# Optimization experiments

Hardware: AMD Instinct MI355X
Metric: run time of the kernel (lower is better)

Reference implementation:

```python
import jax, jax.numpy as jnp
import numpy as np

N, E, D, H, C, HID, ED = 50000, 800000, 128, 8, 16, 512, 32


def setup_inputs() -> dict:
    key = jax.random.key(0)
    ks = jax.random.split(key, 16)
    s = 0.05
    return {
        "h": jax.random.normal(ks[0], (N, D), jnp.float32),
        "edge_index": jax.random.randint(ks[1], (2, E), 0, N, jnp.int64),
        "edge_attr": jax.random.normal(ks[2], (E, ED), jnp.float32),
        "w1": jax.random.normal(ks[3], (D, HID), jnp.float32) * s,
        "b1": jnp.zeros((HID,), jnp.float32),
        "w2": jax.random.normal(ks[4], (HID, D), jnp.float32) * s,
        "b2": jnp.zeros((D,), jnp.float32),
        "ln_g": jnp.ones((D,), jnp.float32),
        "ln_b": jnp.zeros((D,), jnp.float32),
        "Wl": jax.random.normal(ks[5], (D, H * C), jnp.float32) * s,
        "bl": jnp.zeros((H * C,), jnp.float32),
        "Wr": jax.random.normal(ks[6], (D, H * C), jnp.float32) * s,
        "br": jnp.zeros((H * C,), jnp.float32),
        "We": jax.random.normal(ks[7], (ED, H * C), jnp.float32) * s,
        "att": jax.random.normal(ks[8], (H, C), jnp.float32) * s,
        "bias_out": jnp.zeros((H * C,), jnp.float32),
    }


def _layer_norm(x, g, b, eps=1e-5):
    mu = jnp.mean(x, axis=-1, keepdims=True)
    var = jnp.var(x, axis=-1, keepdims=True)
    return (x - mu) * jax.lax.rsqrt(var + eps) * g + b


def reference(h, edge_index, edge_attr, w1, b1, w2, b2, ln_g, ln_b,
              Wl, bl, Wr, br, We, att, bias_out):
    # FFN + residual + LayerNorm (dropout = identity in eval)
    u = jax.nn.relu(h @ w1 + b1) @ w2 + b2
    v = _layer_norm(h + u, ln_g, ln_b)

    src, dst = edge_index[0], edge_index[1]
    # GATv2Conv: separate source/target transforms + edge transform
    xl = (v @ Wl + bl).reshape(N, H, C)
    xr = (v @ Wr + br).reshape(N, H, C)
    xe = (edge_attr @ We).reshape(E, H, C)
    x = jax.nn.leaky_relu(xl[src] + xr[dst] + xe, 0.2)  # [E,H,C]
    logits = jnp.einsum("ehc,hc->eh", x, att)            # [E,H]
    # segment softmax over incoming edges of each destination node
    m = jax.lax.stop_gradient(jax.ops.segment_max(logits, dst, num_segments=N))
    ex = jnp.exp(logits - m[dst])
    den = jax.ops.segment_sum(ex, dst, num_segments=N)
    alpha = ex / den[dst]                                # [E,H]
    msg = xl[src] * alpha[..., None]                     # [E,H,C]
    w = jax.ops.segment_sum(msg, dst, num_segments=N).reshape(N, H * C) + bias_out
    output = _layer_norm(w + v, ln_g, ln_b)
    return output, alpha
```

## Files before the change

kernel.cpp:

```cpp
#include <hip/hip_runtime.h>
#include <math.h>

#define N_NODES 50000
#define E_EDGES 800000
#define D_DIM   128
#define H_HEADS 8
#define C_CH    16
#define HID_DIM 512
#define ED_DIM  32

typedef __attribute__((ext_vector_type(8))) short short8;
typedef __attribute__((ext_vector_type(4))) float f32x4;

__device__ __forceinline__ short f2bf(float f) {
    unsigned u = __float_as_uint(f);
    return (short)((u + 0x7FFFu + ((u >> 16) & 1u)) >> 16);
}
__device__ __forceinline__ float bf2f(short s) {
    return __uint_as_float(((unsigned)(unsigned short)s) << 16);
}

__global__ __launch_bounds__(64) void repack_kernel(
    const float* __restrict__ w1, const float* __restrict__ w2,
    const float* __restrict__ Wl, const float* __restrict__ Wr,
    const float* __restrict__ We,
    short8* __restrict__ w1p, short8* __restrict__ w2p,
    short8* __restrict__ Wlp, short8* __restrict__ Wrp,
    short8* __restrict__ Wep)
{
    int b = blockIdx.x;
    const float* src; short8* dst; int Nw, nc, rel;
    if (b < 128)      { src = w1; dst = w1p; Nw = 512; nc = 4;  rel = b; }
    else if (b < 256) { src = w2; dst = w2p; Nw = 128; nc = 16; rel = b - 128; }
    else if (b < 288) { src = Wl; dst = Wlp; Nw = 128; nc = 4;  rel = b - 256; }
    else if (b < 320) { src = Wr; dst = Wrp; Nw = 128; nc = 4;  rel = b - 288; }
    else              { src = We; dst = Wep; Nw = 128; nc = 1;  rel = b - 320; }
    int t = rel / nc, c = rel % nc;
    int l = threadIdx.x, quad = l >> 4, col = l & 15;
    short8 r;
    #pragma unroll
    for (int j = 0; j < 8; ++j)
        r[j] = f2bf(src[(size_t)(c * 32 + quad * 8 + j) * Nw + t * 16 + col]);
    dst[(size_t)rel * 64 + l] = r;
}

__global__ __launch_bounds__(256) void node_ffn_mfma(
    const float* __restrict__ h,
    const float* __restrict__ b1, const float* __restrict__ b2,
    const float* __restrict__ ln_g, const float* __restrict__ ln_b,
    const float* __restrict__ bl, const float* __restrict__ br,
    const short8* __restrict__ w1p, const short8* __restrict__ w2p,
    const short8* __restrict__ Wlp, const short8* __restrict__ Wrp,
    float* __restrict__ v_out, float* __restrict__ xl_out, float* __restrict__ xr_out)
{
    __shared__ short hid_bf[16 * 520];
    __shared__ float v_s[16 * 132];
    __shared__ short v_bf[16 * 136];

    const int tid = threadIdx.x;
    const int w = tid >> 6, lane = tid & 63;
    const int m = lane & 15, quad = lane >> 4;
    const int n0 = blockIdx.x * 16;

    short8 af[4];
    #pragma unroll
    for (int c = 0; c < 4; ++c) {
        const float* hp = h + (size_t)(n0 + m) * 128 + c * 32 + quad * 8;
        float4 p0 = ((const float4*)hp)[0];
        float4 p1 = ((const float4*)hp)[1];
        short8 a;
        a[0] = f2bf(p0.x); a[1] = f2bf(p0.y); a[2] = f2bf(p0.z); a[3] = f2bf(p0.w);
        a[4] = f2bf(p1.x); a[5] = f2bf(p1.y); a[6] = f2bf(p1.z); a[7] = f2bf(p1.w);
        af[c] = a;
    }

    {
        f32x4 acc[8];
        #pragma unroll
        for (int t = 0; t < 8; ++t) acc[t] = (f32x4){0.f, 0.f, 0.f, 0.f};
        #pragma unroll
        for (int t = 0; t < 8; ++t) {
            int tile = w * 8 + t;
            #pragma unroll
            for (int c = 0; c < 4; ++c) {
                short8 bf = w1p[(size_t)(tile * 4 + c) * 64 + lane];
                acc[t] = __builtin_amdgcn_mfma_f32_16x16x32_bf16(af[c], bf, acc[t], 0, 0, 0);
            }
        }
        #pragma unroll
        for (int t = 0; t < 8; ++t) {
            int col = (w * 8 + t) * 16 + m;
            float bias = b1[col];
            #pragma unroll
            for (int r = 0; r < 4; ++r) {
                int row = quad * 4 + r;
                hid_bf[row * 520 + col] = f2bf(fmaxf(acc[t][r] + bias, 0.f));
            }
        }
    }
    __syncthreads();

    {
        f32x4 acc2[2];
        acc2[0] = (f32x4){0.f, 0.f, 0.f, 0.f};
        acc2[1] = (f32x4){0.f, 0.f, 0.f, 0.f};
        #pragma unroll 4
        for (int c = 0; c < 16; ++c) {
            short8 a = *(const short8*)&hid_bf[m * 520 + c * 32 + quad * 8];
            #pragma unroll
            for (int t = 0; t < 2; ++t) {
                short8 bf = w2p[(size_t)((w * 2 + t) * 16 + c) * 64 + lane];
                acc2[t] = __builtin_amdgcn_mfma_f32_16x16x32_bf16(a, bf, acc2[t], 0, 0, 0);
            }
        }
        #pragma unroll
        for (int t = 0; t < 2; ++t) {
            int col = (w * 2 + t) * 16 + m;
            float bias = b2[col];
            #pragma unroll
            for (int r = 0; r < 4; ++r) {
                int row = quad * 4 + r;
                v_s[row * 132 + col] = acc2[t][r] + bias + h[(size_t)(n0 + row) * 128 + col];
            }
        }
    }
    __syncthreads();

    {
        float g0 = ln_g[lane], g1 = ln_g[lane + 64];
        float be0 = ln_b[lane], be1 = ln_b[lane + 64];
        #pragma unroll
        for (int p = 0; p < 4; ++p) {
            int nd = w * 4 + p;
            float x0 = v_s[nd * 132 + lane], x1 = v_s[nd * 132 + lane + 64];
            float s = x0 + x1, ss = x0 * x0 + x1 * x1;
            #pragma unroll
            for (int off = 1; off < 64; off <<= 1) {
                s  += __shfl_xor(s, off);
                ss += __shfl_xor(ss, off);
            }
            float mu = s * (1.f / 128.f);
            float var = ss * (1.f / 128.f) - mu * mu;
            float rs = rsqrtf(var + 1e-5f);
            float y0 = (x0 - mu) * rs * g0 + be0;
            float y1 = (x1 - mu) * rs * g1 + be1;
            v_out[(size_t)(n0 + nd) * 128 + lane]      = y0;
            v_out[(size_t)(n0 + nd) * 128 + lane + 64] = y1;
            v_bf[nd * 136 + lane]      = f2bf(y0);
            v_bf[nd * 136 + lane + 64] = f2bf(y1);
        }
    }
    __syncthreads();

    {
        short8 af3[4];
        #pragma unroll
        for (int c = 0; c < 4; ++c)
            af3[c] = *(const short8*)&v_bf[m * 136 + c * 32 + quad * 8];
        f32x4 accl[2], accr[2];
        #pragma unroll
        for (int t = 0; t < 2; ++t) {
            accl[t] = (f32x4){0.f, 0.f, 0.f, 0.f};
            accr[t] = (f32x4){0.f, 0.f, 0.f, 0.f};
        }
        #pragma unroll
        for (int t = 0; t < 2; ++t) {
            int tile = w * 2 + t;
            #pragma unroll
            for (int c = 0; c < 4; ++c) {
                accl[t] = __builtin_amdgcn_mfma_f32_16x16x32_bf16(
                    af3[c], Wlp[(size_t)(tile * 4 + c) * 64 + lane], accl[t], 0, 0, 0);
                accr[t] = __builtin_amdgcn_mfma_f32_16x16x32_bf16(
                    af3[c], Wrp[(size_t)(tile * 4 + c) * 64 + lane], accr[t], 0, 0, 0);
            }
        }
        #pragma unroll
        for (int t = 0; t < 2; ++t) {
            int col = (w * 2 + t) * 16 + m;
            float bld = bl[col], brd = br[col];
            #pragma unroll
            for (int r = 0; r < 4; ++r) {
                int row = quad * 4 + r;
                xl_out[(size_t)(n0 + row) * 128 + col] = accl[t][r] + bld;
                xr_out[(size_t)(n0 + row) * 128 + col] = accr[t][r] + brd;
            }
        }
    }
}

__global__ __launch_bounds__(256) void edge_logits_mfma(
    const int* __restrict__ edge_index, const float* __restrict__ edge_attr,
    const short8* __restrict__ Wep, const float* __restrict__ att,
    const float* __restrict__ xl, const float* __restrict__ xr,
    float* __restrict__ logits_out, unsigned* __restrict__ cnt,
    unsigned short* __restrict__ rank)
{
    __shared__ short8 We_f[512];
    __shared__ short xe_s[64 * 136];
    const int tid = threadIdx.x;
    const int w = tid >> 6, lane = tid & 63;
    const int m = lane & 15, quad = lane >> 4;
    const int e0 = blockIdx.x * 64;

    We_f[tid]       = Wep[tid];
    We_f[tid + 256] = Wep[tid + 256];

    const float* eap = edge_attr + (size_t)(e0 + w * 16 + m) * 32 + quad * 8;
    float4 p0 = ((const float4*)eap)[0];
    float4 p1 = ((const float4*)eap)[1];
    short8 a;
    a[0] = f2bf(p0.x); a[1] = f2bf(p0.y); a[2] = f2bf(p0.z); a[3] = f2bf(p0.w);
    a[4] = f2bf(p1.x); a[5] = f2bf(p1.y); a[6] = f2bf(p1.z); a[7] = f2bf(p1.w);

    __syncthreads();

    f32x4 acc[8];
    #pragma unroll
    for (int t = 0; t < 8; ++t) acc[t] = (f32x4){0.f, 0.f, 0.f, 0.f};
    #pragma unroll
    for (int t = 0; t < 8; ++t)
        acc[t] = __builtin_amdgcn_mfma_f32_16x16x32_bf16(a, We_f[t * 64 + lane], acc[t], 0, 0, 0);

    #pragma unroll
    for (int t = 0; t < 8; ++t) {
        #pragma unroll
        for (int r = 0; r < 4; ++r)
            xe_s[(w * 16 + quad * 4 + r) * 136 + t * 16 + m] = f2bf(acc[t][r]);
    }
    __syncthreads();

    const int g = quad;
    const int s = m;
    const int d0 = s * 8;
    float4 at0 = ((const float4*)(att + d0))[0];
    float4 at1 = ((const float4*)(att + d0))[1];

    #pragma unroll
    for (int p = 0; p < 4; ++p) {
        int el = p * 16 + w * 4 + g;
        int e = e0 + el;
        int src = edge_index[e];
        int dst = edge_index[E_EDGES + e];
        const float4* xlp = (const float4*)(xl + (size_t)src * 128 + d0);
        const float4* xrp = (const float4*)(xr + (size_t)dst * 128 + d0);
        float4 a0 = xlp[0], a1 = xlp[1];
        float4 r0 = xrp[0], r1 = xrp[1];
        short8 xe8 = *(const short8*)&xe_s[el * 136 + d0];

        float xv[8] = { a0.x + r0.x + bf2f(xe8[0]), a0.y + r0.y + bf2f(xe8[1]),
                        a0.z + r0.z + bf2f(xe8[2]), a0.w + r0.w + bf2f(xe8[3]),
                        a1.x + r1.x + bf2f(xe8[4]), a1.y + r1.y + bf2f(xe8[5]),
                        a1.z + r1.z + bf2f(xe8[6]), a1.w + r1.w + bf2f(xe8[7]) };
        float atv[8] = { at0.x, at0.y, at0.z, at0.w, at1.x, at1.y, at1.z, at1.w };
        float pq = 0.f;
        #pragma unroll
        for (int dd = 0; dd < 8; ++dd) {
            float x = xv[dd];
            x = (x > 0.f) ? x : 0.2f * x;
            pq += x * atv[dd];
        }
        pq += __shfl_xor(pq, 1);
        if ((s & 1) == 0)
            logits_out[(size_t)e * 8 + (s >> 1)] = pq;
        if (s == 0) {
            unsigned rk = atomicAdd(&cnt[dst], 1u);
            rank[e] = (unsigned short)rk;
        }
    }
}

__global__ __launch_bounds__(1024) void scan_kernel(
    const unsigned* __restrict__ cnt, int* __restrict__ rowstart)
{
    __shared__ int wsum[16];
    __shared__ int s_carry;
    const int t = threadIdx.x, wv = t >> 6, lane = t & 63;
    if (t == 0) s_carry = 0;
    __syncthreads();
    for (int base = 0; base < N_NODES; base += 1024) {
        int i = base + t;
        int v = (i < N_NODES) ? (int)cnt[i] : 0;
        int s = v;
        #pragma unroll
        for (int off = 1; off < 64; off <<= 1) {
            int nb = __shfl_up(s, off);
            if (lane >= off) s += nb;
        }
        if (lane == 63) wsum[wv] = s;
        __syncthreads();
        int woff = s_carry;
        for (int k = 0; k < wv; ++k) woff += wsum[k];
        if (i < N_NODES) rowstart[i] = woff + s - v;
        int tot = woff + s;
        __syncthreads();
        if (t == 1023) s_carry = tot;
    }
}

__global__ __launch_bounds__(256) void scatter_kernel(
    const int* __restrict__ edge_index, const unsigned short* __restrict__ rank,
    const int* __restrict__ rowstart, int* __restrict__ eidx)
{
    int e = blockIdx.x * 256 + threadIdx.x;
    if (e >= E_EDGES) return;
    int dst = edge_index[E_EDGES + e];
    eidx[rowstart[dst] + (int)rank[e]] = e;
}

__global__ __launch_bounds__(256) void node_aggregate_kernel(
    const int* __restrict__ eidx, const int* __restrict__ rowstart,
    const unsigned* __restrict__ cnt, const int* __restrict__ edge_index,
    const float* __restrict__ xl, const float* __restrict__ v,
    const float* __restrict__ bias_out,
    const float* __restrict__ ln_g, const float* __restrict__ ln_b,
    float* __restrict__ alphabuf, float* __restrict__ out)
{
    const int wv = threadIdx.x >> 6, lane = threadIdx.x & 63;
    const int n = blockIdx.x * 4 + wv;
    if (n >= N_NODES) return;
    const int start = rowstart[n];
    const int num = (int)cnt[n];

    const int hh = lane & 7;
    const int slot = lane >> 3;

    float den = 0.f;
    for (int i = slot; i < num; i += 8) {
        int e = eidx[start + i];
        den += expf(alphabuf[(size_t)e * 8 + hh]);
    }
    den += __shfl_xor(den, 8);
    den += __shfl_xor(den, 16);
    den += __shfl_xor(den, 32);
    float inv = 1.f / den;

    const int g = lane >> 4, s = lane & 15;
    const int h3 = s >> 1;
    float iv3 = __shfl(inv, h3);
    float acc[8] = {0.f, 0.f, 0.f, 0.f, 0.f, 0.f, 0.f, 0.f};
    for (int i = 0; i < num; i += 4) {
        int ii = i + g;
        if (ii < num) {
            int e = eidx[start + ii];
            int src = edge_index[e];
            float lg = alphabuf[(size_t)e * 8 + h3];
            float al = expf(lg) * iv3;
            if ((s & 1) == 0) alphabuf[(size_t)e * 8 + h3] = al;
            const float4* xp = (const float4*)(xl + (size_t)src * 128 + s * 8);
            float4 q0 = xp[0], q1 = xp[1];
            acc[0] += q0.x * al; acc[1] += q0.y * al;
            acc[2] += q0.z * al; acc[3] += q0.w * al;
            acc[4] += q1.x * al; acc[5] += q1.y * al;
            acc[6] += q1.z * al; acc[7] += q1.w * al;
        }
    }
    #pragma unroll
    for (int k = 0; k < 8; ++k) {
        acc[k] += __shfl_xor(acc[k], 16);
        acc[k] += __shfl_xor(acc[k], 32);
    }

    const float* vp = v + (size_t)n * 128 + s * 8;
    float4 v0 = ((const float4*)vp)[0], v1 = ((const float4*)vp)[1];
    float4 b0 = ((const float4*)(bias_out + s * 8))[0];
    float4 b1 = ((const float4*)(bias_out + s * 8))[1];
    float x[8];
    x[0] = acc[0] + b0.x + v0.x; x[1] = acc[1] + b0.y + v0.y;
    x[2] = acc[2] + b0.z + v0.z; x[3] = acc[3] + b0.w + v0.w;
    x[4] = acc[4] + b1.x + v1.x; x[5] = acc[5] + b1.y + v1.y;
    x[6] = acc[6] + b1.z + v1.z; x[7] = acc[7] + b1.w + v1.w;
    float sm = 0.f, ssm = 0.f;
    #pragma unroll
    for (int k = 0; k < 8; ++k) { sm += x[k]; ssm += x[k] * x[k]; }
    #pragma unroll
    for (int off = 1; off < 16; off <<= 1) {
        sm  += __shfl_xor(sm, off);
        ssm += __shfl_xor(ssm, off);
    }
    float mu = sm * (1.f / 128.f);
    float var = ssm * (1.f / 128.f) - mu * mu;
    float rs = rsqrtf(var + 1e-5f);
    if (g == 0) {
        float4 g0 = ((const float4*)(ln_g + s * 8))[0];
        float4 g1 = ((const float4*)(ln_g + s * 8))[1];
        float4 be0 = ((const float4*)(ln_b + s * 8))[0];
        float4 be1 = ((const float4*)(ln_b + s * 8))[1];
        float4 o0, o1;
        o0.x = (x[0] - mu) * rs * g0.x + be0.x;
        o0.y = (x[1] - mu) * rs * g0.y + be0.y;
        o0.z = (x[2] - mu) * rs * g0.z + be0.z;
        o0.w = (x[3] - mu) * rs * g0.w + be0.w;
        o1.x = (x[4] - mu) * rs * g1.x + be1.x;
        o1.y = (x[5] - mu) * rs * g1.y + be1.y;
        o1.z = (x[6] - mu) * rs * g1.z + be1.z;
        o1.w = (x[7] - mu) * rs * g1.w + be1.w;
        float4* op = (float4*)(out + (size_t)n * 128 + s * 8);
        op[0] = o0; op[1] = o1;
    }
}

extern "C" void kernel_launch(void* const* d_in, const int* in_sizes, int n_in,
                              void* d_out, int out_size, void* d_ws, size_t ws_size,
                              hipStream_t stream)
{
    const float* h        = (const float*)d_in[0];
    const int*   edge_idx = (const int*)  d_in[1];
    const float* edge_attr= (const float*)d_in[2];
    const float* w1       = (const float*)d_in[3];
    const float* b1       = (const float*)d_in[4];
    const float* w2       = (const float*)d_in[5];
    const float* b2       = (const float*)d_in[6];
    const float* ln_g     = (const float*)d_in[7];
    const float* ln_b     = (const float*)d_in[8];
    const float* Wl       = (const float*)d_in[9];
    const float* bl       = (const float*)d_in[10];
    const float* Wr       = (const float*)d_in[11];
    const float* br       = (const float*)d_in[12];
    const float* We       = (const float*)d_in[13];
    const float* att      = (const float*)d_in[14];
    const float* bias_out = (const float*)d_in[15];

    float* out   = (float*)d_out;
    float* alpha = out + (size_t)N_NODES * 128;

    short8* w1p = (short8*)alpha;
    short8* w2p = w1p + 128 * 64;
    short8* Wlp = w2p + 128 * 64;
    short8* Wrp = Wlp + 32 * 64;

    float*          v        = (float*)d_ws;
    float*          xl       = v  + (size_t)N_NODES * 128;
    float*          xr       = xl + (size_t)N_NODES * 128;
    unsigned*       cnt      = (unsigned*)(xr + (size_t)N_NODES * 128);
    int*            rowstart = (int*)(cnt + N_NODES);
    unsigned short* rank     = (unsigned short*)(rowstart + N_NODES);
    short8*         Wep      = (short8*)(rank + E_EDGES);
    int*            eidx     = (int*)xr;

    hipMemsetAsync(cnt, 0, (size_t)N_NODES * sizeof(unsigned), stream);

    repack_kernel<<<328, 64, 0, stream>>>(w1, w2, Wl, Wr, We,
                                          w1p, w2p, Wlp, Wrp, Wep);
    node_ffn_mfma<<<N_NODES / 16, 256, 0, stream>>>(
        h, b1, b2, ln_g, ln_b, bl, br, w1p, w2p, Wlp, Wrp, v, xl, xr);
    edge_logits_mfma<<<E_EDGES / 64, 256, 0, stream>>>(
        edge_idx, edge_attr, Wep, att, xl, xr, alpha, cnt, rank);
    scan_kernel<<<1, 1024, 0, stream>>>(cnt, rowstart);
    scatter_kernel<<<(E_EDGES + 255) / 256, 256, 0, stream>>>(
        edge_idx, rank, rowstart, eidx);
    node_aggregate_kernel<<<(N_NODES + 3) / 4, 256, 0, stream>>>(
        eidx, rowstart, cnt, edge_idx, xl, v, bias_out, ln_g, ln_b, alpha, out);
}
```

Measured before the change: 528.2 us.

## Build CSR before edge logits and process edges in destination-sorted order

Edge counting moves into a standalone count kernel ahead of the FFN, so the CSR (scan plus scatter) is built before the logits kernel. The logits kernel then walks edges in destination-sorted order using a packed 16-bit src/dst array, which should make the xr[dst] gathers hit cache. The aggregate kernel reads src from the contiguous packed array instead of gathering edge_index by edge id, and the scan now reads cnt four entries at a time. The trade-offs are that edge_attr reads and logit writes become scattered by original edge id, and one extra kernel launch is added.

```diff
diff --git a/kernel.cpp b/kernel.cpp
--- a/kernel.cpp
+++ b/kernel.cpp
@@ -44,6 +44,15 @@
     dst[(size_t)rel * 64 + l] = r;
 }
 
+__global__ __launch_bounds__(256) void count_kernel(
+    const int* __restrict__ edge_index, unsigned* __restrict__ cnt,
+    unsigned short* __restrict__ rank)
+{
+    int e = blockIdx.x * 256 + threadIdx.x;
+    int dst = edge_index[E_EDGES + e];
+    rank[e] = (unsigned short)atomicAdd(&cnt[dst], 1u);
+}
+
 __global__ __launch_bounds__(256) void node_ffn_mfma(
     const float* __restrict__ h,
     const float* __restrict__ b1, const float* __restrict__ b2,
@@ -188,32 +197,90 @@
     }
 }
 
+__global__ __launch_bounds__(1024) void scan_kernel(
+    const unsigned* __restrict__ cnt, int* __restrict__ rowstart)
+{
+    __shared__ int wsum[16];
+    __shared__ int s_carry;
+    const int t = threadIdx.x, wv = t >> 6, lane = t & 63;
+    if (t == 0) s_carry = 0;
+    __syncthreads();
+    for (int b4 = 0; b4 < N_NODES / 4; b4 += 1024) {
+        int i4 = b4 + t;
+        int4 v4 = make_int4(0, 0, 0, 0);
+        if (i4 < N_NODES / 4) v4 = ((const int4*)cnt)[i4];
+        int v = v4.x + v4.y + v4.z + v4.w;
+        int s = v;
+        #pragma unroll
+        for (int off = 1; off < 64; off <<= 1) {
+            int nb = __shfl_up(s, off);
+            if (lane >= off) s += nb;
+        }
+        if (lane == 63) wsum[wv] = s;
+        __syncthreads();
+        int woff = s_carry;
+        for (int k = 0; k < wv; ++k) woff += wsum[k];
+        int tot = woff + s;
+        if (i4 < N_NODES / 4) {
+            int e0 = woff + s - v;
+            int4 r;
+            r.x = e0;
+            r.y = e0 + v4.x;
+            r.z = r.y + v4.y;
+            r.w = r.z + v4.z;
+            ((int4*)rowstart)[i4] = r;
+        }
+        __syncthreads();
+        if (t == 1023) s_carry = tot;
+    }
+}
+
+__global__ __launch_bounds__(256) void scatter_kernel(
+    const int* __restrict__ edge_index, const unsigned short* __restrict__ rank,
+    const int* __restrict__ rowstart, int* __restrict__ eidx,
+    unsigned* __restrict__ srcdst)
+{
+    int e = blockIdx.x * 256 + threadIdx.x;
+    if (e >= E_EDGES) return;
+    int src = edge_index[e];
+    int dst = edge_index[E_EDGES + e];
+    int pos = rowstart[dst] + (int)rank[e];
+    eidx[pos] = e;
+    srcdst[pos] = (unsigned)src | ((unsigned)dst << 16);
+}
+
 __global__ __launch_bounds__(256) void edge_logits_mfma(
-    const int* __restrict__ edge_index, const float* __restrict__ edge_attr,
+    const int* __restrict__ eidx, const unsigned* __restrict__ srcdst,
+    const float* __restrict__ edge_attr,
     const short8* __restrict__ Wep, const float* __restrict__ att,
     const float* __restrict__ xl, const float* __restrict__ xr,
-    float* __restrict__ logits_out, unsigned* __restrict__ cnt,
-    unsigned short* __restrict__ rank)
+    float* __restrict__ logits_out)
 {
     __shared__ short8 We_f[512];
     __shared__ short xe_s[64 * 136];
+    __shared__ int e_s[64];
+    __shared__ unsigned sd_s[64];
     const int tid = threadIdx.x;
     const int w = tid >> 6, lane = tid & 63;
     const int m = lane & 15, quad = lane >> 4;
-    const int e0 = blockIdx.x * 64;
+    const int p0b = blockIdx.x * 64;
 
     We_f[tid]       = Wep[tid];
     We_f[tid + 256] = Wep[tid + 256];
-
-    const float* eap = edge_attr + (size_t)(e0 + w * 16 + m) * 32 + quad * 8;
+    if (tid < 64) {
+        int pos = p0b + tid;
+        e_s[tid]  = eidx[pos];
+        sd_s[tid] = srcdst[pos];
+    }
+    __syncthreads();
+
+    const float* eap = edge_attr + (size_t)e_s[w * 16 + m] * 32 + quad * 8;
     float4 p0 = ((const float4*)eap)[0];
     float4 p1 = ((const float4*)eap)[1];
     short8 a;
     a[0] = f2bf(p0.x); a[1] = f2bf(p0.y); a[2] = f2bf(p0.z); a[3] = f2bf(p0.w);
     a[4] = f2bf(p1.x); a[5] = f2bf(p1.y); a[6] = f2bf(p1.z); a[7] = f2bf(p1.w);
 
-    __syncthreads();
-
     f32x4 acc[8];
     #pragma unroll
     for (int t = 0; t < 8; ++t) acc[t] = (f32x4){0.f, 0.f, 0.f, 0.f};
@@ -238,9 +305,9 @@
     #pragma unroll
     for (int p = 0; p < 4; ++p) {
         int el = p * 16 + w * 4 + g;
-        int e = e0 + el;
-        int src = edge_index[e];
-        int dst = edge_index[E_EDGES + e];
+        unsigned sd = sd_s[el];
+        int src = (int)(sd & 0xffffu);
+        int dst = (int)(sd >> 16);
         const float4* xlp = (const float4*)(xl + (size_t)src * 128 + d0);
         const float4* xrp = (const float4*)(xr + (size_t)dst * 128 + d0);
         float4 a0 = xlp[0], a1 = xlp[1];
@@ -260,56 +327,16 @@
             pq += x * atv[dd];
         }
         pq += __shfl_xor(pq, 1);
-        if ((s & 1) == 0)
+        if ((s & 1) == 0) {
+            int e = e_s[el];
             logits_out[(size_t)e * 8 + (s >> 1)] = pq;
-        if (s == 0) {
-            unsigned rk = atomicAdd(&cnt[dst], 1u);
-            rank[e] = (unsigned short)rk;
-        }
-    }
-}
-
-__global__ __launch_bounds__(1024) void scan_kernel(
-    const unsigned* __restrict__ cnt, int* __restrict__ rowstart)
-{
-    __shared__ int wsum[16];
-    __shared__ int s_carry;
-    const int t = threadIdx.x, wv = t >> 6, lane = t & 63;
-    if (t == 0) s_carry = 0;
-    __syncthreads();
-    for (int base = 0; base < N_NODES; base += 1024) {
-        int i = base + t;
-        int v = (i < N_NODES) ? (int)cnt[i] : 0;
-        int s = v;
-        #pragma unroll
-        for (int off = 1; off < 64; off <<= 1) {
-            int nb = __shfl_up(s, off);
-            if (lane >= off) s += nb;
-        }
-        if (lane == 63) wsum[wv] = s;
-        __syncthreads();
-        int woff = s_carry;
-        for (int k = 0; k < wv; ++k) woff += wsum[k];
-        if (i < N_NODES) rowstart[i] = woff + s - v;
-        int tot = woff + s;
-        __syncthreads();
-        if (t == 1023) s_carry = tot;
-    }
-}
-
-__global__ __launch_bounds__(256) void scatter_kernel(
-    const int* __restrict__ edge_index, const unsigned short* __restrict__ rank,
-    const int* __restrict__ rowstart, int* __restrict__ eidx)
-{
-    int e = blockIdx.x * 256 + threadIdx.x;
-    if (e >= E_EDGES) return;
-    int dst = edge_index[E_EDGES + e];
-    eidx[rowstart[dst] + (int)rank[e]] = e;
+        }
+    }
 }
 
 __global__ __launch_bounds__(256) void node_aggregate_kernel(
     const int* __restrict__ eidx, const int* __restrict__ rowstart,
-    const unsigned* __restrict__ cnt, const int* __restrict__ edge_index,
+    const unsigned* __restrict__ cnt, const unsigned* __restrict__ srcdst,
     const float* __restrict__ xl, const float* __restrict__ v,
     const float* __restrict__ bias_out,
     const float* __restrict__ ln_g, const float* __restrict__ ln_b,
@@ -342,7 +369,7 @@
         int ii = i + g;
         if (ii < num) {
             int e = eidx[start + ii];
-            int src = edge_index[e];
+            int src = (int)(srcdst[start + ii] & 0xffffu);
             float lg = alphabuf[(size_t)e * 8 + h3];
             float al = expf(lg) * iv3;
             if ((s & 1) == 0) alphabuf[(size_t)e * 8 + h3] = al;
@@ -435,19 +462,21 @@
     int*            rowstart = (int*)(cnt + N_NODES);
     unsigned short* rank     = (unsigned short*)(rowstart + N_NODES);
     short8*         Wep      = (short8*)(rank + E_EDGES);
-    int*            eidx     = (int*)xr;
+    int*            eidx     = (int*)(Wep + 512);
+    unsigned*       srcdst   = (unsigned*)(eidx + E_EDGES);
 
     hipMemsetAsync(cnt, 0, (size_t)N_NODES * sizeof(unsigned), stream);
 
     repack_kernel<<<328, 64, 0, stream>>>(w1, w2, Wl, Wr, We,
                                           w1p, w2p, Wlp, Wrp, Wep);
+    count_kernel<<<E_EDGES / 256, 256, 0, stream>>>(edge_idx, cnt, rank);
     node_ffn_mfma<<<N_NODES / 16, 256, 0, stream>>>(
         h, b1, b2, ln_g, ln_b, bl, br, w1p, w2p, Wlp, Wrp, v, xl, xr);
-    edge_logits_mfma<<<E_EDGES / 64, 256, 0, stream>>>(
-        edge_idx, edge_attr, Wep, att, xl, xr, alpha, cnt, rank);
     scan_kernel<<<1, 1024, 0, stream>>>(cnt, rowstart);
     scatter_kernel<<<(E_EDGES + 255) / 256, 256, 0, stream>>>(
-        edge_idx, rank, rowstart, eidx);
+        edge_idx, rank, rowstart, eidx, srcdst);
+    edge_logits_mfma<<<E_EDGES / 64, 256, 0, stream>>>(
+        eidx, srcdst, edge_attr, Wep, att, xl, xr, alpha);
     node_aggregate_kernel<<<(N_NODES + 3) / 4, 256, 0, stream>>>(
-        eidx, rowstart, cnt, edge_idx, xl, v, bias_out, ln_g, ln_b, alpha, out);
-}
+        eidx, rowstart, cnt, srcdst, xl, v, bias_out, ln_g, ln_b, alpha, out);
+}
```

Result: faster. 496.6 us (-6.0%).
